# Performance work log

Hardware: AMD Instinct MI355X
Metric: run time of the kernel (lower is better)

## Reference

```python
import jax, jax.numpy as jnp
import numpy as np

N = 100000   # nodes
E = 5000000  # edges (avg degree 50)
H = 16       # hidden dim


def gcn_conv(x, edge_index, edge_weight, W, b, num_nodes):
    """PyG GCNConv with edge weights: add self-loops (weight 1), symmetric
    normalization deg^-1/2 * w * deg^-1/2, linear transform, scatter-add."""
    row, col = edge_index[0], edge_index[1]  # source j -> target i
    loop = jnp.arange(num_nodes, dtype=edge_index.dtype)
    row = jnp.concatenate([row, loop])
    col = jnp.concatenate([col, loop])
    w = jnp.concatenate([edge_weight, jnp.ones((num_nodes,), edge_weight.dtype)])
    deg = jax.ops.segment_sum(w, col, num_segments=num_nodes)
    dinv = jnp.where(deg > 0, jax.lax.rsqrt(jnp.where(deg > 0, deg, 1.0)), 0.0)
    norm = dinv[row] * w * dinv[col]               # [E+N]
    h = x @ W                                      # [N, out]
    msg = norm[:, None] * h[row]                   # gather + scale
    out = jax.ops.segment_sum(msg, col, num_segments=num_nodes)  # scatter-add
    return out + b


def setup_inputs() -> dict:
    key = jax.random.key(0)
    k = jax.random.split(key, 7)
    x = jax.random.normal(k[0], (N, 1), dtype=jnp.float32)
    edge_index = jax.random.randint(k[1], (2, E), 0, N, dtype=jnp.int32)
    edge_attr = jax.random.uniform(k[2], (E,), dtype=jnp.float32)
    W1 = jax.random.normal(k[3], (1, H), dtype=jnp.float32) * (1.0 / np.sqrt(1.0))
    b1 = jnp.zeros((H,), dtype=jnp.float32)
    W2 = jax.random.normal(k[4], (H, 1), dtype=jnp.float32) * (1.0 / np.sqrt(H))
    b2 = jnp.zeros((1,), dtype=jnp.float32)
    return {"x": x, "edge_index": edge_index, "edge_attr": edge_attr,
            "W1": W1, "b1": b1, "W2": W2, "b2": b2}


def reference(x, edge_index, edge_attr, W1, b1, W2, b2):
    h = gcn_conv(x, edge_index, edge_attr, W1, b1, N)
    h = jax.nn.relu(h)
    out = gcn_conv(h, edge_index, edge_attr, W2, b2, N)
    return out
```

## Files before the change

### kernel.cpp

```cpp
#include <hip/hip_runtime.h>

#define THREADS 256
#define BSHIFT  12
#define BSIZE   4096
#define MAXNB   32
#define M       32
#define CAP     208896
#define EPB     2048
#define EPT     (EPB / THREADS)

__global__ void k_init(int* __restrict__ cur, int nb) {
    int t = threadIdx.x;
    if (t < nb) cur[t] = t * CAP;
}

__global__ void k_scatter(const int* __restrict__ row, const int* __restrict__ col,
                          const float* __restrict__ w, int* __restrict__ cur,
                          int2* __restrict__ rec, int E, int nb) {
    __shared__ int  hist[MAXNB];
    __shared__ int  lofs[MAXNB + 1];
    __shared__ int  rbase[MAXNB];
    __shared__ int2 buf[EPB];
    int t = threadIdx.x;
    if (t < MAXNB) hist[t] = 0;
    __syncthreads();
    int base = blockIdx.x * EPB;
    bool full = (base + EPB <= E);

    if (full) {
#pragma unroll
        for (int k = 0; k < EPT / 4; ++k) {
            int4 c = *(const int4*)(col + base + (t + k * THREADS) * 4);
            atomicAdd(&hist[c.x >> BSHIFT], 1);
            atomicAdd(&hist[c.y >> BSHIFT], 1);
            atomicAdd(&hist[c.z >> BSHIFT], 1);
            atomicAdd(&hist[c.w >> BSHIFT], 1);
        }
    } else {
        for (int k = 0; k < EPT; ++k) {
            int e = base + t + k * THREADS;
            if (e < E) atomicAdd(&hist[col[e] >> BSHIFT], 1);
        }
    }
    __syncthreads();
    if (t == 0) {
        int s = 0;
        for (int b = 0; b < nb; ++b) { lofs[b] = s; s += hist[b]; }
        lofs[nb] = s;
    }
    if (t < nb) rbase[t] = hist[t] ? atomicAdd(&cur[t], hist[t]) : 0;
    __syncthreads();
    if (t < MAXNB) hist[t] = 0;
    __syncthreads();

    if (full) {
#pragma unroll
        for (int k = 0; k < EPT / 4; ++k) {
            int idx = base + (t + k * THREADS) * 4;
            int4   c  = *(const int4*)(col + idx);
            int4   r  = *(const int4*)(row + idx);
            float4 wv = *(const float4*)(w + idx);
            int b, rk;
            b = c.x >> BSHIFT; rk = atomicAdd(&hist[b], 1);
            buf[lofs[b] + rk] = make_int2(((c.x & (BSIZE-1)) << 17) | r.x, __float_as_int(wv.x));
            b = c.y >> BSHIFT; rk = atomicAdd(&hist[b], 1);
            buf[lofs[b] + rk] = make_int2(((c.y & (BSIZE-1)) << 17) | r.y, __float_as_int(wv.y));
            b = c.z >> BSHIFT; rk = atomicAdd(&hist[b], 1);
            buf[lofs[b] + rk] = make_int2(((c.z & (BSIZE-1)) << 17) | r.z, __float_as_int(wv.z));
            b = c.w >> BSHIFT; rk = atomicAdd(&hist[b], 1);
            buf[lofs[b] + rk] = make_int2(((c.w & (BSIZE-1)) << 17) | r.w, __float_as_int(wv.w));
        }
    } else {
        for (int k = 0; k < EPT; ++k) {
            int e = base + t + k * THREADS;
            if (e < E) {
                int c = col[e];
                int b = c >> BSHIFT;
                int rk = atomicAdd(&hist[b], 1);
                buf[lofs[b] + rk] = make_int2(((c & (BSIZE-1)) << 17) | row[e],
                                              __float_as_int(w[e]));
            }
        }
    }
    __syncthreads();

    int total = lofs[nb];
    for (int j = t; j < total; j += THREADS) {
        int lo = 0, hi = nb;
        while (hi - lo > 1) { int mid = (lo + hi) >> 1; if (lofs[mid] <= j) lo = mid; else hi = mid; }
        rec[rbase[lo] + (j - lofs[lo])] = buf[j];
    }
}

template <bool HAS_SRC>
__global__ void k_acc(const int2* __restrict__ rec, const int* __restrict__ cur,
                      const float* __restrict__ src, float* __restrict__ part) {
    __shared__ float acc[BSIZE];
    int b = blockIdx.x / M, m = blockIdx.x % M;
    for (int j = threadIdx.x; j < BSIZE; j += THREADS) acc[j] = 0.0f;
    __syncthreads();
    int s = b * CAP;
    int c = cur[b] - s;
    int chunk = (((c + M - 1) / M) + 3) & ~3;
    int lo = s + m * chunk;
    int hi = min(s + c, lo + chunk);
    const int4* rec4 = (const int4*)rec;
    int i = lo + threadIdx.x * 4;
    for (; i + 3 < hi; i += THREADS * 4) {
        int4 a = rec4[i >> 1];
        int4 d = rec4[(i >> 1) + 1];
        float v0 = __int_as_float(a.y), v1 = __int_as_float(a.w);
        float v2 = __int_as_float(d.y), v3 = __int_as_float(d.w);
        if (HAS_SRC) {
            v0 *= src[a.x & 0x1FFFF];
            v1 *= src[a.z & 0x1FFFF];
            v2 *= src[d.x & 0x1FFFF];
            v3 *= src[d.z & 0x1FFFF];
        }
        atomicAdd(&acc[((unsigned)a.x) >> 17], v0);
        atomicAdd(&acc[((unsigned)a.z) >> 17], v1);
        atomicAdd(&acc[((unsigned)d.x) >> 17], v2);
        atomicAdd(&acc[((unsigned)d.z) >> 17], v3);
    }
    for (; i < hi; ++i) {
        int2 r = rec[i];
        float v = __int_as_float(r.y);
        if (HAS_SRC) v *= src[r.x & 0x1FFFF];
        atomicAdd(&acc[((unsigned)r.x) >> 17], v);
    }
    __syncthreads();
    float* dst = part + (size_t)blockIdx.x * BSIZE;
    for (int j = threadIdx.x; j < BSIZE; j += THREADS) dst[j] = acc[j];
}

__device__ __forceinline__ float reduceM(const float* __restrict__ part, int n) {
    int b = n >> BSHIFT, ofs = n & (BSIZE - 1);
    const float* pp = part + (size_t)b * M * BSIZE + ofs;
    float s = 0.0f;
#pragma unroll
    for (int m = 0; m < M; ++m) s += pp[(size_t)m * BSIZE];
    return s;
}

__global__ void k_red_dinv(const float* __restrict__ part, const float* __restrict__ x,
                           float* __restrict__ dinv, float* __restrict__ p, int N) {
    int i = blockIdx.x * blockDim.x + threadIdx.x;
    if (i < N) {
        float d  = reduceM(part, i) + 1.0f;
        float di = rsqrtf(d);
        dinv[i] = di;
        p[i] = di * x[i];
    }
}

__global__ void k_red_mlp(const float* __restrict__ part, const float* __restrict__ dinv,
                          const float* __restrict__ p,
                          const float* __restrict__ W1, const float* __restrict__ b1,
                          const float* __restrict__ W2,
                          float* __restrict__ q, int N) {
    int i = blockIdx.x * blockDim.x + threadIdx.x;
    if (i < N) {
        float di = dinv[i];
        float s  = di * reduceM(part, i) + di * p[i];
        float acc = 0.0f;
#pragma unroll
        for (int k = 0; k < 16; ++k) {
            float h = fmaxf(s * W1[k] + b1[k], 0.0f);
            acc += h * W2[k];
        }
        q[i] = di * acc;
    }
}

__global__ void k_red_out(const float* __restrict__ part, const float* __restrict__ dinv,
                          const float* __restrict__ q, const float* __restrict__ b2,
                          float* __restrict__ out, int N) {
    int i = blockIdx.x * blockDim.x + threadIdx.x;
    if (i < N) {
        float di = dinv[i];
        out[i] = di * reduceM(part, i) + di * q[i] + b2[0];
    }
}

extern "C" void kernel_launch(void* const* d_in, const int* in_sizes, int n_in,
                              void* d_out, int out_size, void* d_ws, size_t ws_size,
                              hipStream_t stream) {
    const float* x  = (const float*)d_in[0];
    const int*   ei = (const int*)  d_in[1];
    const float* ew = (const float*)d_in[2];
    const float* W1 = (const float*)d_in[3];
    const float* b1 = (const float*)d_in[4];
    const float* W2 = (const float*)d_in[5];
    const float* b2 = (const float*)d_in[6];

    const int N = in_sizes[0];
    const int E = in_sizes[2];
    const int* row = ei;
    const int* col = ei + E;
    const int nb = (N + BSIZE - 1) >> BSHIFT;

    char* wsp = (char*)d_ws;
    int2*  rec  = (int2*)wsp;                          wsp += (size_t)nb * CAP * 8;
    float* part = (float*)wsp;                         wsp += (size_t)nb * M * BSIZE * 4;
    float* dinv = (float*)wsp;                         wsp += (size_t)N * 4;
    float* p    = (float*)wsp;                         wsp += (size_t)N * 4;
    float* q    = (float*)wsp;                         wsp += (size_t)N * 4;
    int*   cur  = (int*)wsp;

    float* out = (float*)d_out;

    const int eb  = (E + EPB - 1) / EPB;
    const int nbk = (N + THREADS - 1) / THREADS;
    const int ab  = nb * M;

    k_init   <<<1, 64, 0, stream>>>(cur, nb);
    k_scatter<<<eb, THREADS, 0, stream>>>(row, col, ew, cur, rec, E, nb);

    k_acc<false><<<ab, THREADS, 0, stream>>>(rec, cur, nullptr, part);
    k_red_dinv  <<<nbk, THREADS, 0, stream>>>(part, x, dinv, p, N);

    k_acc<true><<<ab, THREADS, 0, stream>>>(rec, cur, p, part);
    k_red_mlp  <<<nbk, THREADS, 0, stream>>>(part, dinv, p, W1, b1, W2, q, N);

    k_acc<true><<<ab, THREADS, 0, stream>>>(rec, cur, q, part);
    k_red_out  <<<nbk, THREADS, 0, stream>>>(part, dinv, q, b2, out, N);
}
```

Measured before the change: 247.9 us.

## Replace fixed-capacity bucket bins with two-pass count/scan/scatter over replicated counters

The single-pass bucket scatter used one global atomic cursor per destination bucket with a fixed per-bucket capacity. It is replaced by a counting pass that spreads atomics over 64 replicas per bucket, a scan that computes compact 4-aligned start offsets, and a scatter pass that reuses the per-block histogram. The scatter stores a per-slot bucket id so the write-out loop no longer binary-searches, and the accumulate kernel walks two replica cells per block with 8-wide unrolled loads. The aim is less contention on global cursors and less search overhead, at the cost of an extra kernel launch, a single-block scan and reading col twice.

New measurement: 241.6 us. 1.03x faster.

```diff
diff --git a/kernel.cpp b/kernel.cpp
--- a/kernel.cpp
+++ b/kernel.cpp
@@ -5,28 +5,18 @@
 #define BSIZE   4096
 #define MAXNB   32
 #define M       32
-#define CAP     208896
+#define NREP    64
 #define EPB     2048
 #define EPT     (EPB / THREADS)
 
-__global__ void k_init(int* __restrict__ cur, int nb) {
-    int t = threadIdx.x;
-    if (t < nb) cur[t] = t * CAP;
-}
-
-__global__ void k_scatter(const int* __restrict__ row, const int* __restrict__ col,
-                          const float* __restrict__ w, int* __restrict__ cur,
-                          int2* __restrict__ rec, int E, int nb) {
-    __shared__ int  hist[MAXNB];
-    __shared__ int  lofs[MAXNB + 1];
-    __shared__ int  rbase[MAXNB];
-    __shared__ int2 buf[EPB];
+__global__ void k_count(const int* __restrict__ col, int* __restrict__ cur,
+                        int2* __restrict__ hr, int E, int nb) {
+    __shared__ int hist[MAXNB];
     int t = threadIdx.x;
     if (t < MAXNB) hist[t] = 0;
     __syncthreads();
     int base = blockIdx.x * EPB;
     bool full = (base + EPB <= E);
-
     if (full) {
 #pragma unroll
         for (int k = 0; k < EPT / 4; ++k) {
@@ -43,16 +33,66 @@
         }
     }
     __syncthreads();
-    if (t == 0) {
-        int s = 0;
-        for (int b = 0; b < nb; ++b) { lofs[b] = s; s += hist[b]; }
-        lofs[nb] = s;
-    }
-    if (t < nb) rbase[t] = hist[t] ? atomicAdd(&cur[t], hist[t]) : 0;
-    __syncthreads();
-    if (t < MAXNB) hist[t] = 0;
-    __syncthreads();
-
+    int rep = blockIdx.x & (NREP - 1);
+    if (t < nb) {
+        int rel = atomicAdd(&cur[t * NREP + rep], hist[t]);
+        hr[blockIdx.x * MAXNB + t] = make_int2(hist[t], rel);
+    }
+}
+
+__global__ void k_scan(const int* __restrict__ cnt, int* __restrict__ starts, int n) {
+    __shared__ int tsum[THREADS];
+    int t = threadIdx.x;
+    int per = (n + THREADS - 1) / THREADS;
+    int lo = t * per, hi = min(n, lo + per);
+    int s = 0;
+    for (int i = lo; i < hi; ++i) s += (cnt[i] + 3) & ~3;
+    tsum[t] = s;
+    __syncthreads();
+    for (int d = 1; d < THREADS; d <<= 1) {
+        int v = (t >= d) ? tsum[t - d] : 0;
+        __syncthreads();
+        tsum[t] += v;
+        __syncthreads();
+    }
+    int base = (t > 0) ? tsum[t - 1] : 0;
+    for (int i = lo; i < hi; ++i) { starts[i] = base; base += (cnt[i] + 3) & ~3; }
+}
+
+__global__ void k_scatter(const int* __restrict__ row, const int* __restrict__ col,
+                          const float* __restrict__ w,
+                          const int2* __restrict__ hr, const int* __restrict__ starts,
+                          int2* __restrict__ rec, int E, int nb) {
+    __shared__ int  lofs[MAXNB + 1];
+    __shared__ int  rank[MAXNB];
+    __shared__ int  rbase[MAXNB];
+    __shared__ int2 buf[EPB];
+    __shared__ unsigned char bkt[EPB];
+    int t = threadIdx.x;
+    if (t < MAXNB) rank[t] = 0;
+    int rep = blockIdx.x & (NREP - 1);
+    if (t < 64) {
+        int h = 0, rel = 0;
+        if (t < nb) {
+            int2 v = hr[blockIdx.x * MAXNB + t];
+            h = v.x; rel = v.y;
+        }
+        int inc = h;
+#pragma unroll
+        for (int d = 1; d < 32; d <<= 1) {
+            int o = __shfl_up(inc, d, 64);
+            if (t >= d) inc += o;
+        }
+        if (t == 0) lofs[0] = 0;
+        if (t < nb) {
+            lofs[t + 1] = inc;
+            rbase[t] = starts[t * NREP + rep] + rel;
+        }
+    }
+    __syncthreads();
+
+    int base = blockIdx.x * EPB;
+    bool full = (base + EPB <= E);
     if (full) {
 #pragma unroll
         for (int k = 0; k < EPT / 4; ++k) {
@@ -60,15 +100,19 @@
             int4   c  = *(const int4*)(col + idx);
             int4   r  = *(const int4*)(row + idx);
             float4 wv = *(const float4*)(w + idx);
-            int b, rk;
-            b = c.x >> BSHIFT; rk = atomicAdd(&hist[b], 1);
-            buf[lofs[b] + rk] = make_int2(((c.x & (BSIZE-1)) << 17) | r.x, __float_as_int(wv.x));
-            b = c.y >> BSHIFT; rk = atomicAdd(&hist[b], 1);
-            buf[lofs[b] + rk] = make_int2(((c.y & (BSIZE-1)) << 17) | r.y, __float_as_int(wv.y));
-            b = c.z >> BSHIFT; rk = atomicAdd(&hist[b], 1);
-            buf[lofs[b] + rk] = make_int2(((c.z & (BSIZE-1)) << 17) | r.z, __float_as_int(wv.z));
-            b = c.w >> BSHIFT; rk = atomicAdd(&hist[b], 1);
-            buf[lofs[b] + rk] = make_int2(((c.w & (BSIZE-1)) << 17) | r.w, __float_as_int(wv.w));
+            int b, rk, pos;
+            b = c.x >> BSHIFT; rk = atomicAdd(&rank[b], 1); pos = lofs[b] + rk;
+            buf[pos] = make_int2(((c.x & (BSIZE-1)) << 17) | r.x, __float_as_int(wv.x));
+            bkt[pos] = (unsigned char)b;
+            b = c.y >> BSHIFT; rk = atomicAdd(&rank[b], 1); pos = lofs[b] + rk;
+            buf[pos] = make_int2(((c.y & (BSIZE-1)) << 17) | r.y, __float_as_int(wv.y));
+            bkt[pos] = (unsigned char)b;
+            b = c.z >> BSHIFT; rk = atomicAdd(&rank[b], 1); pos = lofs[b] + rk;
+            buf[pos] = make_int2(((c.z & (BSIZE-1)) << 17) | r.z, __float_as_int(wv.z));
+            bkt[pos] = (unsigned char)b;
+            b = c.w >> BSHIFT; rk = atomicAdd(&rank[b], 1); pos = lofs[b] + rk;
+            buf[pos] = make_int2(((c.w & (BSIZE-1)) << 17) | r.w, __float_as_int(wv.w));
+            bkt[pos] = (unsigned char)b;
         }
     } else {
         for (int k = 0; k < EPT; ++k) {
@@ -76,9 +120,10 @@
             if (e < E) {
                 int c = col[e];
                 int b = c >> BSHIFT;
-                int rk = atomicAdd(&hist[b], 1);
-                buf[lofs[b] + rk] = make_int2(((c & (BSIZE-1)) << 17) | row[e],
-                                              __float_as_int(w[e]));
+                int rk = atomicAdd(&rank[b], 1);
+                int pos = lofs[b] + rk;
+                buf[pos] = make_int2(((c & (BSIZE-1)) << 17) | row[e], __float_as_int(w[e]));
+                bkt[pos] = (unsigned char)b;
             }
         }
     }
@@ -86,47 +131,56 @@
 
     int total = lofs[nb];
     for (int j = t; j < total; j += THREADS) {
-        int lo = 0, hi = nb;
-        while (hi - lo > 1) { int mid = (lo + hi) >> 1; if (lofs[mid] <= j) lo = mid; else hi = mid; }
-        rec[rbase[lo] + (j - lofs[lo])] = buf[j];
+        int b = bkt[j];
+        rec[rbase[b] + (j - lofs[b])] = buf[j];
     }
 }
 
 template <bool HAS_SRC>
-__global__ void k_acc(const int2* __restrict__ rec, const int* __restrict__ cur,
-                      const float* __restrict__ src, float* __restrict__ part) {
+__global__ void k_acc(const int2* __restrict__ rec, const int* __restrict__ cnt,
+                      const int* __restrict__ starts, const float* __restrict__ src,
+                      float* __restrict__ part) {
     __shared__ float acc[BSIZE];
     int b = blockIdx.x / M, m = blockIdx.x % M;
     for (int j = threadIdx.x; j < BSIZE; j += THREADS) acc[j] = 0.0f;
     __syncthreads();
-    int s = b * CAP;
-    int c = cur[b] - s;
-    int chunk = (((c + M - 1) / M) + 3) & ~3;
-    int lo = s + m * chunk;
-    int hi = min(s + c, lo + chunk);
     const int4* rec4 = (const int4*)rec;
-    int i = lo + threadIdx.x * 4;
-    for (; i + 3 < hi; i += THREADS * 4) {
-        int4 a = rec4[i >> 1];
-        int4 d = rec4[(i >> 1) + 1];
-        float v0 = __int_as_float(a.y), v1 = __int_as_float(a.w);
-        float v2 = __int_as_float(d.y), v3 = __int_as_float(d.w);
-        if (HAS_SRC) {
-            v0 *= src[a.x & 0x1FFFF];
-            v1 *= src[a.z & 0x1FFFF];
-            v2 *= src[d.x & 0x1FFFF];
-            v3 *= src[d.z & 0x1FFFF];
-        }
-        atomicAdd(&acc[((unsigned)a.x) >> 17], v0);
-        atomicAdd(&acc[((unsigned)a.z) >> 17], v1);
-        atomicAdd(&acc[((unsigned)d.x) >> 17], v2);
-        atomicAdd(&acc[((unsigned)d.z) >> 17], v3);
-    }
-    for (; i < hi; ++i) {
-        int2 r = rec[i];
-        float v = __int_as_float(r.y);
-        if (HAS_SRC) v *= src[r.x & 0x1FFFF];
-        atomicAdd(&acc[((unsigned)r.x) >> 17], v);
+#pragma unroll
+    for (int rr = 0; rr < NREP / M; ++rr) {
+        int cell = b * NREP + m * (NREP / M) + rr;
+        int lo = starts[cell];
+        int hi = lo + cnt[cell];
+        int i = lo + threadIdx.x * 8;
+        for (; i + 7 < hi; i += THREADS * 8) {
+            int4 q0 = rec4[(i >> 1) + 0];
+            int4 q1 = rec4[(i >> 1) + 1];
+            int4 q2 = rec4[(i >> 1) + 2];
+            int4 q3 = rec4[(i >> 1) + 3];
+            float v0 = __int_as_float(q0.y), v1 = __int_as_float(q0.w);
+            float v2 = __int_as_float(q1.y), v3 = __int_as_float(q1.w);
+            float v4 = __int_as_float(q2.y), v5 = __int_as_float(q2.w);
+            float v6 = __int_as_float(q3.y), v7 = __int_as_float(q3.w);
+            if (HAS_SRC) {
+                v0 *= src[q0.x & 0x1FFFF]; v1 *= src[q0.z & 0x1FFFF];
+                v2 *= src[q1.x & 0x1FFFF]; v3 *= src[q1.z & 0x1FFFF];
+                v4 *= src[q2.x & 0x1FFFF]; v5 *= src[q2.z & 0x1FFFF];
+                v6 *= src[q3.x & 0x1FFFF]; v7 *= src[q3.z & 0x1FFFF];
+            }
+            atomicAdd(&acc[((unsigned)q0.x) >> 17], v0);
+            atomicAdd(&acc[((unsigned)q0.z) >> 17], v1);
+            atomicAdd(&acc[((unsigned)q1.x) >> 17], v2);
+            atomicAdd(&acc[((unsigned)q1.z) >> 17], v3);
+            atomicAdd(&acc[((unsigned)q2.x) >> 17], v4);
+            atomicAdd(&acc[((unsigned)q2.z) >> 17], v5);
+            atomicAdd(&acc[((unsigned)q3.x) >> 17], v6);
+            atomicAdd(&acc[((unsigned)q3.z) >> 17], v7);
+        }
+        for (; i < hi; ++i) {
+            int2 r = rec[i];
+            float v = __int_as_float(r.y);
+            if (HAS_SRC) v *= src[r.x & 0x1FFFF];
+            atomicAdd(&acc[((unsigned)r.x) >> 17], v);
+        }
     }
     __syncthreads();
     float* dst = part + (size_t)blockIdx.x * BSIZE;
@@ -198,30 +252,35 @@
     const int* row = ei;
     const int* col = ei + E;
     const int nb = (N + BSIZE - 1) >> BSHIFT;
+    const int eb = (E + EPB - 1) / EPB;
 
     char* wsp = (char*)d_ws;
-    int2*  rec  = (int2*)wsp;                          wsp += (size_t)nb * CAP * 8;
-    float* part = (float*)wsp;                         wsp += (size_t)nb * M * BSIZE * 4;
-    float* dinv = (float*)wsp;                         wsp += (size_t)N * 4;
-    float* p    = (float*)wsp;                         wsp += (size_t)N * 4;
-    float* q    = (float*)wsp;                         wsp += (size_t)N * 4;
-    int*   cur  = (int*)wsp;
+    int2*  rec    = (int2*)wsp;   wsp += (size_t)E * 8 + 65536;
+    float* part   = (float*)wsp;  wsp += (size_t)nb * M * BSIZE * 4;
+    float* dinv   = (float*)wsp;  wsp += (size_t)N * 4;
+    float* p      = (float*)wsp;  wsp += (size_t)N * 4;
+    float* q      = (float*)wsp;  wsp += (size_t)N * 4;
+    int2*  hr     = (int2*)wsp;   wsp += (size_t)eb * MAXNB * 8;
+    int*   cur    = (int*)wsp;    wsp += (size_t)nb * NREP * 4;
+    int*   starts = (int*)wsp;
 
     float* out = (float*)d_out;
 
-    const int eb  = (E + EPB - 1) / EPB;
     const int nbk = (N + THREADS - 1) / THREADS;
     const int ab  = nb * M;
 
-    k_init   <<<1, 64, 0, stream>>>(cur, nb);
-    k_scatter<<<eb, THREADS, 0, stream>>>(row, col, ew, cur, rec, E, nb);
-
-    k_acc<false><<<ab, THREADS, 0, stream>>>(rec, cur, nullptr, part);
+    hipMemsetAsync(cur, 0, (size_t)nb * NREP * sizeof(int), stream);
+
+    k_count  <<<eb, THREADS, 0, stream>>>(col, cur, hr, E, nb);
+    k_scan   <<<1, THREADS, 0, stream>>>(cur, starts, nb * NREP);
+    k_scatter<<<eb, THREADS, 0, stream>>>(row, col, ew, hr, starts, rec, E, nb);
+
+    k_acc<false><<<ab, THREADS, 0, stream>>>(rec, cur, starts, nullptr, part);
     k_red_dinv  <<<nbk, THREADS, 0, stream>>>(part, x, dinv, p, N);
 
-    k_acc<true><<<ab, THREADS, 0, stream>>>(rec, cur, p, part);
+    k_acc<true><<<ab, THREADS, 0, stream>>>(rec, cur, starts, p, part);
     k_red_mlp  <<<nbk, THREADS, 0, stream>>>(part, dinv, p, W1, b1, W2, q, N);
 
-    k_acc<true><<<ab, THREADS, 0, stream>>>(rec, cur, q, part);
+    k_acc<true><<<ab, THREADS, 0, stream>>>(rec, cur, starts, q, part);
     k_red_out  <<<nbk, THREADS, 0, stream>>>(part, dinv, q, b2, out, N);
 }
```
